# Kernel tuning notes

Hardware: AMD Instinct MI355X
Metric: run time of the kernel (lower is better)

## Reference

```python
import jax, jax.numpy as jnp
import numpy as np

B, S, D = 8, 1024, 1024
H = 16
DH = D // H
DFF = 4096
L = 2
EPS = 1e-6


def setup_inputs() -> dict:
    key = jax.random.key(0)
    ks = jax.random.split(key, 12)
    sc = 0.02
    x = jax.random.normal(ks[0], (B, S, D), dtype=jnp.float32)
    # causal mask: 1 where position j > i (masked), broadcast over batch/head
    mask = jnp.triu(jnp.ones((S, S), dtype=jnp.float32), k=1)[None, None]
    Wq = jax.random.normal(ks[1], (L, D, D), dtype=jnp.float32) * sc
    Wk = jax.random.normal(ks[2], (L, D, D), dtype=jnp.float32) * sc
    Wv = jax.random.normal(ks[3], (L, D, D), dtype=jnp.float32) * sc
    Wo = jax.random.normal(ks[4], (L, D, D), dtype=jnp.float32) * sc
    bq = jnp.zeros((L, D), jnp.float32)
    bk = jnp.zeros((L, D), jnp.float32)
    bv = jnp.zeros((L, D), jnp.float32)
    bo = jnp.zeros((L, D), jnp.float32)
    W1 = jax.random.normal(ks[5], (L, D, DFF), dtype=jnp.float32) * sc
    b1 = jnp.zeros((L, DFF), jnp.float32)
    W2 = jax.random.normal(ks[6], (L, DFF, D), dtype=jnp.float32) * sc
    b2 = jnp.zeros((L, D), jnp.float32)
    ln1_g = jnp.ones((L, D), jnp.float32)
    ln1_b = jnp.zeros((L, D), jnp.float32)
    ln2_g = jnp.ones((L, D), jnp.float32)
    ln2_b = jnp.zeros((L, D), jnp.float32)
    return dict(x=x, mask=mask, Wq=Wq, bq=bq, Wk=Wk, bk=bk, Wv=Wv, bv=bv,
                Wo=Wo, bo=bo, W1=W1, b1=b1, W2=W2, b2=b2,
                ln1_g=ln1_g, ln1_b=ln1_b, ln2_g=ln2_g, ln2_b=ln2_b)


def layer_norm(x, g, b):
    mu = jnp.mean(x, axis=-1, keepdims=True)
    var = jnp.mean(jnp.square(x - mu), axis=-1, keepdims=True)
    return (x - mu) * jax.lax.rsqrt(var + EPS) * g + b


def reference(x, mask, Wq, bq, Wk, bk, Wv, bv, Wo, bo, W1, b1, W2, b2,
              ln1_g, ln1_b, ln2_g, ln2_b):
    scale = 1.0 / jnp.sqrt(jnp.float32(DH))
    for l in range(L):
        # --- multi-head attention (inference mode: no dropout) ---
        q = (x @ Wq[l] + bq[l]).reshape(B, S, H, DH).transpose(0, 2, 1, 3)
        k = (x @ Wk[l] + bk[l]).reshape(B, S, H, DH).transpose(0, 2, 1, 3)
        v = (x @ Wv[l] + bv[l]).reshape(B, S, H, DH).transpose(0, 2, 1, 3)
        sim = jnp.einsum('bhqd,bhkd->bhqk', q, k) * scale + mask * (-1e9)
        attn = jax.nn.softmax(sim, axis=-1)
        o = jnp.einsum('bhqk,bhkd->bhqd', attn, v)
        o = o.transpose(0, 2, 1, 3).reshape(B, S, D)
        o = o @ Wo[l] + bo[l]
        x = layer_norm(o + x, ln1_g[l], ln1_b[l])
        # --- feed-forward network ---
        h = jax.nn.relu(x @ W1[l] + b1[l])
        f = h @ W2[l] + b2[l]
        x = layer_norm(x + f, ln2_g[l], ln2_b[l])
    return x
```

## Files before the change

kernel.cpp:

```cpp
#include <hip/hip_runtime.h>

typedef __attribute__((ext_vector_type(8))) short bf16x8;
typedef __attribute__((ext_vector_type(4))) float f32x4;
typedef unsigned short ushort_t;
typedef unsigned int uint32;

#define DEV __device__ __forceinline__

DEV ushort_t f2bf(float f) {
    uint32 u = __float_as_uint(f);
    uint32 r = (u + 0x7FFFu + ((u >> 16) & 1u)) >> 16;
    return (ushort_t)r;
}
DEV float bf2f(ushort_t h) { return __uint_as_float(((uint32)h) << 16); }

#define MFMA16(a, b, c) __builtin_amdgcn_mfma_f32_16x16x32_bf16((a), (b), (c), 0, 0, 0)

DEV void gload_lds16(const void* g, void* l) {
    __builtin_amdgcn_global_load_lds((const __attribute__((address_space(1))) void*)g,
                                     (__attribute__((address_space(3))) void*)l,
                                     16, 0, 0);
}

__global__ __launch_bounds__(256) void init_x(const float* __restrict__ xin,
                                              ushort_t* __restrict__ xr, int n4) {
    int i = blockIdx.x * 256 + threadIdx.x;
    if (i >= n4) return;
    float4 v = ((const float4*)xin)[i];
    ushort4 h;
    h.x = f2bf(v.x); h.y = f2bf(v.y); h.z = f2bf(v.z); h.w = f2bf(v.w);
    ((ushort4*)xr)[i] = h;
}

__global__ __launch_bounds__(256) void transpose_all(const float* __restrict__ Wq,
                                                     const float* __restrict__ Wk,
                                                     const float* __restrict__ Wv,
                                                     const float* __restrict__ Wo,
                                                     const float* __restrict__ W1,
                                                     const float* __restrict__ W2,
                                                     ushort_t* __restrict__ wqkvT,
                                                     ushort_t* __restrict__ woT,
                                                     ushort_t* __restrict__ w1T,
                                                     ushort_t* __restrict__ w2T) {
    const int l = blockIdx.y;
    const int t = blockIdx.x;
    const float* src;
    ushort_t* dst;
    int K, N, ktile, ntile;
    if (t < 4096) {
        const int which = t >> 10, tile = t & 1023;
        K = 1024; N = 1024; ktile = tile >> 5; ntile = tile & 31;
        const size_t o1 = (size_t)l * 1048576;
        if (which == 0)      { src = Wq + o1; dst = wqkvT + (size_t)l * 3145728; }
        else if (which == 1) { src = Wk + o1; dst = wqkvT + (size_t)l * 3145728 + 1048576; }
        else if (which == 2) { src = Wv + o1; dst = wqkvT + (size_t)l * 3145728 + 2097152; }
        else                 { src = Wo + o1; dst = woT + o1; }
    } else if (t < 8192) {
        const int tile = t - 4096;
        K = 1024; N = 4096; ktile = tile >> 7; ntile = tile & 127;
        src = W1 + (size_t)l * 4194304; dst = w1T + (size_t)l * 4194304;
    } else {
        const int tile = t - 8192;
        K = 4096; N = 1024; ktile = tile >> 5; ntile = tile & 31;
        src = W2 + (size_t)l * 4194304; dst = w2T + (size_t)l * 4194304;
    }
    __shared__ float tilebuf[32][33];
    const int tx = threadIdx.x, ty = threadIdx.y;
    const int nt = ntile * 32, kt = ktile * 32;
#pragma unroll
    for (int j = 0; j < 4; ++j)
        tilebuf[ty + j * 8][tx] = src[(size_t)(kt + ty + j * 8) * N + nt + tx];
    __syncthreads();
#pragma unroll
    for (int j = 0; j < 4; ++j)
        dst[(size_t)(nt + ty + j * 8) * K + kt + tx] = f2bf(tilebuf[tx][ty + j * 8]);
}

template <int BM, int MODE, int RELU>
__global__ __launch_bounds__(512, 2) void gemm8p(const ushort_t* __restrict__ A,
                                                 const ushort_t* __restrict__ BT,
                                                 const float* __restrict__ bias,
                                                 void* __restrict__ Cout,
                                                 int M, int N, int K, int gx,
                                                 ushort_t* __restrict__ qout,
                                                 ushort_t* __restrict__ kout,
                                                 ushort_t* __restrict__ vtout,
                                                 const float* __restrict__ bq,
                                                 const float* __restrict__ bk,
                                                 const float* __restrict__ bv) {
    constexpr int AH = BM / 128;
    constexpr int MREP = BM / 32;
    constexpr int PHASES = (BM == 128) ? 2 : 4;
    constexpr int MPP = MREP / PHASES;
    __shared__ ushort_t lds[2][(BM + 256) * 64];

    const int nwg = gridDim.x;
    const int q8 = nwg >> 3, r8 = nwg & 7;
    const int xcd = blockIdx.x & 7, idx = blockIdx.x >> 3;
    const int swz = (xcd < r8 ? xcd * (q8 + 1) : r8 * (q8 + 1) + (xcd - r8) * q8) + idx;
    const int gchunk = gx * 8;
    const int grp = swz / gchunk, rem = swz % gchunk;
    const int byi = grp * 8 + (rem & 7);
    const int bxi = rem >> 3;

    const int tid = threadIdx.x;
    const int w = tid >> 6, lane = tid & 63;
    const int wr = w >> 2, wc = w & 3;
    const int lr = lane & 15, lh = lane >> 4;
    const int row0 = byi * BM, col0 = bxi * 256;

    f32x4 acc[MREP][4] = {};

    const ushort_t* __restrict__ Ab = A + (size_t)row0 * K;
    const ushort_t* __restrict__ Bb = BT + (size_t)col0 * K;
    const int nt = K >> 6;

    const int r8l = lane >> 3;
    const int cu = (lane & 7) ^ r8l;
    const int so = w * 1024 + lane * 8;

    const ushort_t* aS[AH][2];
    const ushort_t* bS[2][2];
#pragma unroll
    for (int h2 = 0; h2 < AH; ++h2)
#pragma unroll
        for (int i = 0; i < 2; ++i)
            aS[h2][i] = Ab + (size_t)(h2 * 128 + (w * 2 + i) * 8 + r8l) * K + cu * 8;
#pragma unroll
    for (int h2 = 0; h2 < 2; ++h2)
#pragma unroll
        for (int i = 0; i < 2; ++i)
            bS[h2][i] = Bb + (size_t)(h2 * 128 + (w * 2 + i) * 8 + r8l) * K + cu * 8;

    auto stageA = [&](int buf, int h2) {
#pragma unroll
        for (int i = 0; i < 2; ++i) {
            gload_lds16(aS[h2][i], &lds[buf][h2 * 8192 + so + i * 512]);
            aS[h2][i] += 64;
        }
    };
    auto stageB = [&](int buf, int h2) {
#pragma unroll
        for (int i = 0; i < 2; ++i) {
            gload_lds16(bS[h2][i], &lds[buf][BM * 64 + h2 * 8192 + so + i * 512]);
            bS[h2][i] += 64;
        }
    };

    int boff[4][2];
#pragma unroll
    for (int ni = 0; ni < 4; ++ni) {
        const int br = wc * 64 + ni * 16 + lr;
        const int rr = br & 127, bh2 = br >> 7;
#pragma unroll
        for (int ks = 0; ks < 2; ++ks)
            boff[ni][ks] = BM * 64 + bh2 * 8192 + rr * 64 + (((ks * 4 + lh) ^ (rr & 7)) * 8);
    }
    int aoff[MREP][2];
#pragma unroll
    for (int mi = 0; mi < MREP; ++mi) {
        const int fr = wr * (BM / 2) + mi * 16 + lr;
        const int rr = fr & 127, fh = fr >> 7;
#pragma unroll
        for (int ks = 0; ks < 2; ++ks)
            aoff[mi][ks] = fh * 8192 + rr * 64 + (((ks * 4 + lh) ^ (rr & 7)) * 8);
    }

    stageB(0, 0); stageB(0, 1);
    stageA(0, 0); if (AH == 2) stageA(0, 1);
    stageB(1, 0); stageB(1, 1);
    asm volatile("s_waitcnt vmcnt(4)" ::: "memory");
    __builtin_amdgcn_sched_barrier(0);
    __builtin_amdgcn_s_barrier();

    for (int t2 = 0; t2 < nt; t2 += 2) {
#pragma unroll
        for (int ti = 0; ti < 2; ++ti) {
            const int t = t2 + ti;
            bf16x8 bfrag[4][2];
#pragma unroll
            for (int p = 0; p < PHASES; ++p) {
                if (p == 0) {
#pragma unroll
                    for (int ni = 0; ni < 4; ++ni)
#pragma unroll
                        for (int ks = 0; ks < 2; ++ks)
                            bfrag[ni][ks] = *(const bf16x8*)&lds[ti][boff[ni][ks]];
                }
                bf16x8 af[MPP][2];
#pragma unroll
                for (int mm = 0; mm < MPP; ++mm)
#pragma unroll
                    for (int ks = 0; ks < 2; ++ks)
                        af[mm][ks] = *(const bf16x8*)&lds[ti][aoff[p * MPP + mm][ks]];
                if (PHASES == 4) {
                    if (p == 0) { if (t + 1 < nt) stageA(1 - ti, 0); }
                    else if (p == 1) { if (AH == 2 && t + 1 < nt) stageA(1 - ti, 1); }
                    else if (p == 2) { if (t + 2 < nt) stageB(ti, 0); }
                    else {
                        if (t + 2 < nt) {
                            stageB(ti, 1);
                            asm volatile("s_waitcnt vmcnt(4)" ::: "memory");
                        } else if (t + 1 < nt) {
                            asm volatile("s_waitcnt vmcnt(0)" ::: "memory");
                        }
                    }
                } else {
                    if (p == 0) { if (t + 1 < nt) stageA(1 - ti, 0); }
                    else {
                        if (t + 2 < nt) {
                            stageB(ti, 0);
                            stageB(ti, 1);
                            asm volatile("s_waitcnt vmcnt(4)" ::: "memory");
                        } else if (t + 1 < nt) {
                            asm volatile("s_waitcnt vmcnt(0)" ::: "memory");
                        }
                    }
                }
                __builtin_amdgcn_sched_barrier(0);
                __builtin_amdgcn_s_barrier();
                asm volatile("s_waitcnt lgkmcnt(0)" ::: "memory");
                __builtin_amdgcn_sched_barrier(0);
                __builtin_amdgcn_s_setprio(1);
#pragma unroll
                for (int mm = 0; mm < MPP; ++mm)
#pragma unroll
                    for (int ni = 0; ni < 4; ++ni)
#pragma unroll
                        for (int ks = 0; ks < 2; ++ks)
                            acc[p * MPP + mm][ni] = MFMA16(af[mm][ks], bfrag[ni][ks], acc[p * MPP + mm][ni]);
                __builtin_amdgcn_s_setprio(0);
                __builtin_amdgcn_sched_barrier(0);
                __builtin_amdgcn_s_barrier();
            }
        }
    }
    (void)M;

    if (MODE == 2 && col0 >= 2048) {
        ushort_t* vb = &lds[0][0] + w * 4096;
        const int hglob = (col0 - 2048 + wc * 64) >> 6;
        const int bidx = row0 >> 10;
        const int srow0 = (row0 & 1023) + wr * 64;
#pragma unroll
        for (int mi = 0; mi < MREP; ++mi) {
#pragma unroll
            for (int ni = 0; ni < 4; ++ni) {
                const int dd = ni * 16 + lr;
                const float bvv = bv[(hglob << 6) + dd];
                ushort4 h4;
                h4.x = f2bf(acc[mi][ni][0] + bvv);
                h4.y = f2bf(acc[mi][ni][1] + bvv);
                h4.z = f2bf(acc[mi][ni][2] + bvv);
                h4.w = f2bf(acc[mi][ni][3] + bvv);
                const int sb = mi * 32 + lh * 8;
                *(ushort4*)((char*)vb + dd * 128 + (sb ^ ((dd & 3) << 4))) = h4;
            }
        }
        const int ddl = lane >> 3, s8 = lane & 7;
#pragma unroll
        for (int j = 0; j < 8; ++j) {
            const int dd = j * 8 + ddl;
            bf16x8 rowv = *(const bf16x8*)((char*)vb + dd * 128 + ((s8 * 16) ^ ((dd & 3) << 4)));
            *(bf16x8*)&vtout[(((size_t)(bidx * 16 + hglob) * 64 + dd) << 10) + srow0 + s8 * 8] = rowv;
        }
    } else {
#pragma unroll
        for (int mi = 0; mi < MREP; ++mi) {
#pragma unroll
            for (int ni = 0; ni < 4; ++ni) {
                const int col = col0 + wc * 64 + ni * 16 + lr;
                const int rowb = row0 + wr * (BM / 2) + mi * 16 + lh * 4;
                if (MODE == 2) {
                    if (col < 1024) {
                        const float bvv = bq[col];
#pragma unroll
                        for (int r = 0; r < 4; ++r)
                            qout[(size_t)(rowb + r) * 1024 + col] = f2bf((acc[mi][ni][r] + bvv) * 0.125f);
                    } else {
                        const int c = col - 1024;
                        const float bvv = bk[c];
#pragma unroll
                        for (int r = 0; r < 4; ++r)
                            kout[(size_t)(rowb + r) * 1024 + c] = f2bf(acc[mi][ni][r] + bvv);
                    }
                } else {
                    const float bvv = bias[col];
#pragma unroll
                    for (int r = 0; r < 4; ++r) {
                        float val = acc[mi][ni][r] + bvv;
                        if (RELU) val = fmaxf(val, 0.f);
                        ((ushort_t*)Cout)[(size_t)(rowb + r) * N + col] = f2bf(val);
                    }
                }
            }
        }
    }
}

__global__ __launch_bounds__(256) void attn_kernel(const ushort_t* __restrict__ q,
                                                   const ushort_t* __restrict__ k,
                                                   const ushort_t* __restrict__ vt,
                                                   ushort_t* __restrict__ o) {
    __shared__ ushort_t ktile[128 * 64];
    __shared__ ushort_t vtile[64 * 128];
    __shared__ ushort_t p_lds[4][16 * 128];

    const int bh = blockIdx.x;
    const int b = bh >> 4, h = bh & 15;
    const int qt = blockIdx.y;
    const int tid = threadIdx.x, w = tid >> 6, lane = tid & 63;
    const int lr = lane & 15, lh = lane >> 4;
    const int qbase = qt * 64 + w * 16;
    const size_t headoff = (size_t)b * 1024 * 1024 + h * 64;
    const size_t vhead = (size_t)(b * 16 + h) << 16;

    bf16x8 qf[2];
#pragma unroll
    for (int ks = 0; ks < 2; ++ks)
        qf[ks] = *(const bf16x8*)&q[headoff + (size_t)(qbase + lr) * 1024 + ks * 32 + lh * 8];

    f32x4 oacc[4] = {};
    float m[4] = {-INFINITY, -INFINITY, -INFINITY, -INFINITY};
    float ls[4] = {0.f, 0.f, 0.f, 0.f};

    const int srow = tid >> 3;
    const int scol8 = (tid & 7) * 8;
    char* const kbase = (char*)ktile;
    char* const vbase = (char*)vtile;
    const int kswzb = (scol8 * 2) ^ ((srow & 7) << 4);
    const int vswzr = ((srow & 15) << 4);
    const ushort_t* kg = k + headoff + (size_t)srow * 1024 + scol8;
    const ushort_t* vg = vt + vhead + (size_t)srow * 1024 + scol8;

    const int jmaxw = qbase + 15;
    const int jend = qt * 64 + 63;

    bf16x8 sk[4], sv[4];
#pragma unroll
    for (int p = 0; p < 4; ++p) sk[p] = *(const bf16x8*)&kg[(size_t)(p * 32) * 1024];
#pragma unroll
    for (int p = 0; p < 2; ++p)
#pragma unroll
        for (int kh = 0; kh < 2; ++kh)
            sv[p * 2 + kh] = *(const bf16x8*)&vg[(size_t)(p * 32) * 1024 + kh * 64];

    for (int j0 = 0; j0 <= jend; j0 += 128) {
        __syncthreads();
#pragma unroll
        for (int p = 0; p < 4; ++p)
            *(bf16x8*)(kbase + (srow + 32 * p) * 128 + kswzb) = sk[p];
#pragma unroll
        for (int p = 0; p < 2; ++p)
#pragma unroll
            for (int kh = 0; kh < 2; ++kh)
                *(bf16x8*)(vbase + (srow + 32 * p) * 256 + ((kh * 128 + scol8 * 2) ^ vswzr)) = sv[p * 2 + kh];
        __syncthreads();
        if (j0 + 128 <= jend) {
#pragma unroll
            for (int p = 0; p < 4; ++p)
                sk[p] = *(const bf16x8*)&kg[(size_t)(j0 + 128 + p * 32) * 1024];
#pragma unroll
            for (int p = 0; p < 2; ++p)
#pragma unroll
                for (int kh = 0; kh < 2; ++kh)
                    sv[p * 2 + kh] = *(const bf16x8*)&vg[(size_t)(p * 32) * 1024 + j0 + 128 + kh * 64];
        }

        if (j0 <= jmaxw) {
            f32x4 s[8] = {};
#pragma unroll
            for (int kt = 0; kt < 8; ++kt) {
                const int krow = kt * 16 + lr;
                const int rswz = ((krow & 7) << 4);
#pragma unroll
                for (int ks = 0; ks < 2; ++ks) {
                    bf16x8 kf = *(const bf16x8*)(kbase + krow * 128 + ((ks * 64 + lh * 16) ^ rswz));
                    s[kt] = MFMA16(qf[ks], kf, s[kt]);
                }
            }
            if (j0 + 127 > qbase) {
#pragma unroll
                for (int kt = 0; kt < 8; ++kt)
#pragma unroll
                    for (int r = 0; r < 4; ++r)
                        s[kt][r] = ((j0 + kt * 16 + lr) <= (qbase + lh * 4 + r)) ? s[kt][r] : -1e9f;
            }
#pragma unroll
            for (int r = 0; r < 4; ++r) {
                float pm = fmaxf(fmaxf(fmaxf(s[0][r], s[1][r]), fmaxf(s[2][r], s[3][r])),
                                 fmaxf(fmaxf(s[4][r], s[5][r]), fmaxf(s[6][r], s[7][r])));
                pm = fmaxf(pm, __shfl_xor(pm, 1, 16));
                pm = fmaxf(pm, __shfl_xor(pm, 2, 16));
                pm = fmaxf(pm, __shfl_xor(pm, 4, 16));
                pm = fmaxf(pm, __shfl_xor(pm, 8, 16));
                const float mn = fmaxf(m[r], pm);
                const float corr = __expf(m[r] - mn);
                m[r] = mn;
                float ps = 0.f;
#pragma unroll
                for (int kt = 0; kt < 8; ++kt) {
                    const float pv = __expf(s[kt][r] - mn);
                    s[kt][r] = pv;
                    ps += pv;
                }
                ps += __shfl_xor(ps, 1, 16);
                ps += __shfl_xor(ps, 2, 16);
                ps += __shfl_xor(ps, 4, 16);
                ps += __shfl_xor(ps, 8, 16);
                ls[r] = ls[r] * corr + ps;
                oacc[0][r] *= corr; oacc[1][r] *= corr;
                oacc[2][r] *= corr; oacc[3][r] *= corr;
            }
            char* const pb = (char*)p_lds[w];
#pragma unroll
            for (int r = 0; r < 4; ++r) {
                const int qrow = lh * 4 + r;
                const int qswz = ((qrow & 15) << 4);
#pragma unroll
                for (int kt = 0; kt < 8; ++kt)
                    *(ushort_t*)(pb + qrow * 256 + ((kt * 32 + lr * 2) ^ qswz)) = f2bf(s[kt][r]);
            }
            const int pswz = ((lr & 15) << 4);
            bf16x8 pa[4];
#pragma unroll
            for (int ks = 0; ks < 4; ++ks)
                pa[ks] = *(const bf16x8*)(pb + lr * 256 + ((ks * 64 + lh * 16) ^ pswz));
#pragma unroll
            for (int dt = 0; dt < 4; ++dt) {
                const int vrow = dt * 16 + lr;
                const int vswz = ((vrow & 15) << 4);
#pragma unroll
                for (int ks = 0; ks < 4; ++ks) {
                    bf16x8 vf = *(const bf16x8*)(vbase + vrow * 256 + ((ks * 64 + lh * 16) ^ vswz));
                    oacc[dt] = MFMA16(pa[ks], vf, oacc[dt]);
                }
            }
        }
    }

    float inv[4];
#pragma unroll
    for (int r = 0; r < 4; ++r) inv[r] = 1.f / ls[r];
#pragma unroll
    for (int dt = 0; dt < 4; ++dt)
#pragma unroll
        for (int r = 0; r < 4; ++r) {
            const int row = qbase + lh * 4 + r;
            o[headoff + (size_t)row * 1024 + dt * 16 + lr] = f2bf(oacc[dt][r] * inv[r]);
        }
}

template <int LAST>
__global__ __launch_bounds__(256) void add_ln(const ushort_t* __restrict__ t,
                                              ushort_t* __restrict__ xr,
                                              const float* __restrict__ g,
                                              const float* __restrict__ bb,
                                              float* __restrict__ out) {
    const int row = blockIdx.x, tid = threadIdx.x;
    const int lane = tid & 63, w = tid >> 6;
    const size_t base = (size_t)row * 1024;
    ushort4 tv = ((const ushort4*)(t + base))[tid];
    ushort4 xv = ((const ushort4*)(xr + base))[tid];
    float v0 = bf2f(tv.x) + bf2f(xv.x), v1 = bf2f(tv.y) + bf2f(xv.y);
    float v2 = bf2f(tv.z) + bf2f(xv.z), v3 = bf2f(tv.w) + bf2f(xv.w);
    float s = v0 + v1 + v2 + v3;
    float sq = v0 * v0 + v1 * v1 + v2 * v2 + v3 * v3;
#pragma unroll
    for (int off = 32; off >= 1; off >>= 1) {
        s += __shfl_xor(s, off);
        sq += __shfl_xor(sq, off);
    }
    __shared__ float red[8];
    if (lane == 0) { red[w] = s; red[4 + w] = sq; }
    __syncthreads();
    s = red[0] + red[1] + red[2] + red[3];
    sq = red[4] + red[5] + red[6] + red[7];
    const float mu = s * (1.f / 1024.f);
    const float var = sq * (1.f / 1024.f) - mu * mu;
    const float rs = rsqrtf(var + 1e-6f);
    float4 gv = ((const float4*)g)[tid];
    float4 bv = ((const float4*)bb)[tid];
    float y0 = (v0 - mu) * rs * gv.x + bv.x;
    float y1 = (v1 - mu) * rs * gv.y + bv.y;
    float y2 = (v2 - mu) * rs * gv.z + bv.z;
    float y3 = (v3 - mu) * rs * gv.w + bv.w;
    if (LAST) {
        float4 yo; yo.x = y0; yo.y = y1; yo.z = y2; yo.w = y3;
        ((float4*)(out + base))[tid] = yo;
    } else {
        ushort4 hh;
        hh.x = f2bf(y0); hh.y = f2bf(y1); hh.z = f2bf(y2); hh.w = f2bf(y3);
        ((ushort4*)(xr + base))[tid] = hh;
    }
}

extern "C" void kernel_launch(void* const* d_in, const int* in_sizes, int n_in,
                              void* d_out, int out_size, void* d_ws, size_t ws_size,
                              hipStream_t stream) {
    (void)in_sizes; (void)n_in; (void)out_size; (void)ws_size;
    const int B = 8, S = 1024, D = 1024, DFF = 4096, L = 2;
    const int M = B * S;

    const float* x_in = (const float*)d_in[0];
    const float* Wq = (const float*)d_in[2];
    const float* bq = (const float*)d_in[3];
    const float* Wk = (const float*)d_in[4];
    const float* bk = (const float*)d_in[5];
    const float* Wv = (const float*)d_in[6];
    const float* bv = (const float*)d_in[7];
    const float* Wo = (const float*)d_in[8];
    const float* bo = (const float*)d_in[9];
    const float* W1 = (const float*)d_in[10];
    const float* b1 = (const float*)d_in[11];
    const float* W2 = (const float*)d_in[12];
    const float* b2 = (const float*)d_in[13];
    const float* ln1g = (const float*)d_in[14];
    const float* ln1b = (const float*)d_in[15];
    const float* ln2g = (const float*)d_in[16];
    const float* ln2b = (const float*)d_in[17];

    float* out = (float*)d_out;
    char* ws = (char*)d_ws;
    const size_t MB = 1024 * 1024;
    ushort_t* wqkvT = (ushort_t*)(ws + 0 * MB);
    ushort_t* woT = (ushort_t*)(ws + 12 * MB);
    ushort_t* w1T = (ushort_t*)(ws + 16 * MB);
    ushort_t* w2T = (ushort_t*)(ws + 32 * MB);
    ushort_t* xr  = (ushort_t*)(ws + 48 * MB);
    ushort_t* qb  = (ushort_t*)(ws + 64 * MB);
    ushort_t* kb  = (ushort_t*)(ws + 80 * MB);
    ushort_t* vtb = (ushort_t*)(ws + 96 * MB);
    ushort_t* ob  = (ushort_t*)(ws + 112 * MB);
    ushort_t* hb  = (ushort_t*)(ws + 64 * MB);
    ushort_t* tb  = (ushort_t*)(ws + 128 * MB);

    init_x<<<M * D / 4 / 256, 256, 0, stream>>>(x_in, xr, M * D / 4);
    transpose_all<<<dim3(12288, L), dim3(32, 8), 0, stream>>>(
        Wq, Wk, Wv, Wo, W1, W2, wqkvT, woT, w1T, w2T);

    for (int l = 0; l < L; ++l) {
        const size_t wOff = (size_t)l * D * D;
        const size_t bOff = (size_t)l * D;
        gemm8p<128, 2, 0><<<dim3(768), 512, 0, stream>>>(
            xr, wqkvT + (size_t)l * 3 * D * D, nullptr, nullptr, M, 3 * D, D, 12,
            qb, kb, vtb, bq + bOff, bk + bOff, bv + bOff);
        attn_kernel<<<dim3(B * 16, S / 64), 256, 0, stream>>>(qb, kb, vtb, ob);
        gemm8p<128, 1, 0><<<dim3(256), 512, 0, stream>>>(
            ob, woT + wOff, bo + bOff, tb, M, D, D, 4,
            nullptr, nullptr, nullptr, nullptr, nullptr, nullptr);
        add_ln<0><<<M, 256, 0, stream>>>(tb, xr, ln1g + bOff, ln1b + bOff, nullptr);
        gemm8p<256, 1, 1><<<dim3(512), 512, 0, stream>>>(
            xr, w1T + (size_t)l * D * DFF, b1 + (size_t)l * DFF, hb, M, DFF, D, 16,
            nullptr, nullptr, nullptr, nullptr, nullptr, nullptr);
        gemm8p<128, 1, 0><<<dim3(256), 512, 0, stream>>>(
            hb, w2T + (size_t)l * DFF * D, b2 + bOff, tb, M, D, DFF, 4,
            nullptr, nullptr, nullptr, nullptr, nullptr, nullptr);
        if (l == L - 1)
            add_ln<1><<<M, 256, 0, stream>>>(tb, xr, ln2g + bOff, ln2b + bOff, out);
        else
            add_ln<0><<<M, 256, 0, stream>>>(tb, xr, ln2g + bOff, ln2b + bOff, nullptr);
    }
}
```

Measured before the change: 656.4 us.

## Restructure GEMM main loop to simple double-buffered prefetch with k-split phases

Replaces the phased pipeline, where B tiles were prefetched two steps ahead and interleaved with A loads, with a simpler double buffer. Each step now loads the next A and B tiles into the other buffer and waits on vmcnt(0) at the end of the step. For BM=256 the work is split by k-substep instead of by row groups, and A and B stages are issued in separate phases. This reduces wait-count complexity and register pressure but shortens how far ahead loads are issued, so more global latency may be exposed.

```diff
diff --git a/kernel.cpp b/kernel.cpp
--- a/kernel.cpp
+++ b/kernel.cpp
@@ -90,8 +90,6 @@
                                                  const float* __restrict__ bv) {
     constexpr int AH = BM / 128;
     constexpr int MREP = BM / 32;
-    constexpr int PHASES = (BM == 128) ? 2 : 4;
-    constexpr int MPP = MREP / PHASES;
     __shared__ ushort_t lds[2][(BM + 256) * 64];
 
     const int nwg = gridDim.x;
@@ -168,8 +166,7 @@
 
     stageB(0, 0); stageB(0, 1);
     stageA(0, 0); if (AH == 2) stageA(0, 1);
-    stageB(1, 0); stageB(1, 1);
-    asm volatile("s_waitcnt vmcnt(4)" ::: "memory");
+    asm volatile("s_waitcnt vmcnt(0)" ::: "memory");
     __builtin_amdgcn_sched_barrier(0);
     __builtin_amdgcn_s_barrier();
 
@@ -177,45 +174,22 @@
 #pragma unroll
         for (int ti = 0; ti < 2; ++ti) {
             const int t = t2 + ti;
-            bf16x8 bfrag[4][2];
-#pragma unroll
-            for (int p = 0; p < PHASES; ++p) {
-                if (p == 0) {
-#pragma unroll
-                    for (int ni = 0; ni < 4; ++ni)
-#pragma unroll
-                        for (int ks = 0; ks < 2; ++ks)
-                            bfrag[ni][ks] = *(const bf16x8*)&lds[ti][boff[ni][ks]];
-                }
-                bf16x8 af[MPP][2];
-#pragma unroll
-                for (int mm = 0; mm < MPP; ++mm)
+            if (BM == 128) {
+                bf16x8 bfr[2][4], af[4][2];
+#pragma unroll
+                for (int ni = 0; ni < 4; ++ni)
 #pragma unroll
                     for (int ks = 0; ks < 2; ++ks)
-                        af[mm][ks] = *(const bf16x8*)&lds[ti][aoff[p * MPP + mm][ks]];
-                if (PHASES == 4) {
-                    if (p == 0) { if (t + 1 < nt) stageA(1 - ti, 0); }
-                    else if (p == 1) { if (AH == 2 && t + 1 < nt) stageA(1 - ti, 1); }
-                    else if (p == 2) { if (t + 2 < nt) stageB(ti, 0); }
-                    else {
-                        if (t + 2 < nt) {
-                            stageB(ti, 1);
-                            asm volatile("s_waitcnt vmcnt(4)" ::: "memory");
-                        } else if (t + 1 < nt) {
-                            asm volatile("s_waitcnt vmcnt(0)" ::: "memory");
-                        }
-                    }
-                } else {
-                    if (p == 0) { if (t + 1 < nt) stageA(1 - ti, 0); }
-                    else {
-                        if (t + 2 < nt) {
-                            stageB(ti, 0);
-                            stageB(ti, 1);
-                            asm volatile("s_waitcnt vmcnt(4)" ::: "memory");
-                        } else if (t + 1 < nt) {
-                            asm volatile("s_waitcnt vmcnt(0)" ::: "memory");
-                        }
-                    }
+                        bfr[ks][ni] = *(const bf16x8*)&lds[ti][boff[ni][ks]];
+#pragma unroll
+                for (int mm = 0; mm < 4; ++mm)
+#pragma unroll
+                    for (int ks = 0; ks < 2; ++ks)
+                        af[mm][ks] = *(const bf16x8*)&lds[ti][aoff[mm][ks]];
+                if (t + 1 < nt) {
+                    stageA(1 - ti, 0);
+                    stageB(1 - ti, 0);
+                    stageB(1 - ti, 1);
                 }
                 __builtin_amdgcn_sched_barrier(0);
                 __builtin_amdgcn_s_barrier();
@@ -223,15 +197,48 @@
                 __builtin_amdgcn_sched_barrier(0);
                 __builtin_amdgcn_s_setprio(1);
 #pragma unroll
-                for (int mm = 0; mm < MPP; ++mm)
+                for (int mm = 0; mm < 4; ++mm)
 #pragma unroll
                     for (int ni = 0; ni < 4; ++ni)
 #pragma unroll
                         for (int ks = 0; ks < 2; ++ks)
-                            acc[p * MPP + mm][ni] = MFMA16(af[mm][ks], bfrag[ni][ks], acc[p * MPP + mm][ni]);
+                            acc[mm][ni] = MFMA16(af[mm][ks], bfr[ks][ni], acc[mm][ni]);
                 __builtin_amdgcn_s_setprio(0);
+                if (t + 1 < nt)
+                    asm volatile("s_waitcnt vmcnt(0)" ::: "memory");
                 __builtin_amdgcn_sched_barrier(0);
                 __builtin_amdgcn_s_barrier();
+            } else {
+#pragma unroll
+                for (int p = 0; p < 2; ++p) {
+                    bf16x8 bfr[4], af[8];
+#pragma unroll
+                    for (int ni = 0; ni < 4; ++ni)
+                        bfr[ni] = *(const bf16x8*)&lds[ti][boff[ni][p]];
+#pragma unroll
+                    for (int mi = 0; mi < 8; ++mi)
+                        af[mi] = *(const bf16x8*)&lds[ti][aoff[mi][p]];
+                    if (p == 0) {
+                        if (t + 1 < nt) { stageA(1 - ti, 0); stageA(1 - ti, 1); }
+                    } else {
+                        if (t + 1 < nt) { stageB(1 - ti, 0); stageB(1 - ti, 1); }
+                    }
+                    __builtin_amdgcn_sched_barrier(0);
+                    __builtin_amdgcn_s_barrier();
+                    asm volatile("s_waitcnt lgkmcnt(0)" ::: "memory");
+                    __builtin_amdgcn_sched_barrier(0);
+                    __builtin_amdgcn_s_setprio(1);
+#pragma unroll
+                    for (int mi = 0; mi < 8; ++mi)
+#pragma unroll
+                        for (int ni = 0; ni < 4; ++ni)
+                            acc[mi][ni] = MFMA16(af[mi], bfr[ni], acc[mi][ni]);
+                    __builtin_amdgcn_s_setprio(0);
+                    if (p == 1 && t + 1 < nt)
+                        asm volatile("s_waitcnt vmcnt(0)" ::: "memory");
+                    __builtin_amdgcn_sched_barrier(0);
+                    __builtin_amdgcn_s_barrier();
+                }
             }
         }
     }
```

Result: slower. 722.3 us (+10.0%).
